# Kernel tuning notes

Hardware: AMD Instinct MI355X
Metric: run time of the kernel (lower is better)

Reference implementation:

```python
import jax, jax.numpy as jnp
import numpy as np

H = 256          # hidden_size
TH_X = 0.05      # delta threshold on inputs
TH_H = 0.05      # delta threshold on hidden state
F_IN = 6         # engineered feature count


def hardswish(v):
    return v * jnp.clip(v + 3.0, 0.0, 6.0) / 6.0


def setup_inputs() -> dict:
    key = jax.random.key(0)
    ks = jax.random.split(key, 6)
    B, T = 32, 4096
    x = jax.random.normal(ks[0], (B, T, 2), dtype=jnp.float32)
    # x2h: Linear(6, 3H, bias=False) -> weight (3H, 6)
    Wx = jax.random.normal(ks[1], (3 * H, F_IN), dtype=jnp.float32) * (1.0 / np.sqrt(F_IN))
    # h2h: Linear(H, 3H, bias=False) -> weight (3H, H)
    Wh = jax.random.normal(ks[2], (3 * H, H), dtype=jnp.float32) * (1.0 / np.sqrt(H))
    # fc_out: Linear(H, 2, bias=False)
    Wo = jax.random.normal(ks[3], (2, H), dtype=jnp.float32) * (1.0 / np.sqrt(H))
    # tcn conv1: Conv1d(2, 3, k=3, padding=16, dilation=16, bias=False) -> (O,I,K)=(3,2,3)
    Wc1 = jax.random.normal(ks[4], (3, 2, 3), dtype=jnp.float32) * 0.3
    # tcn conv2: Conv1d(3, 2, k=1) -> (2,3,1)
    Wc2 = jax.random.normal(ks[5], (2, 3, 1), dtype=jnp.float32) * 0.3
    return {"x": x, "Wx": Wx, "Wh": Wh, "Wo": Wo, "Wc1": Wc1, "Wc2": Wc2}


def _delta_gru(feats_TBF, Wx, Wh):
    # feats_TBF: (T, B, 6). Initial states are always zeros (the torch module
    # resets them whenever x_p_0 is None, which DeltaGRUModel always passes).
    T, B, F = feats_TBF.shape
    dt = feats_TBF.dtype
    carry0 = (
        jnp.zeros((B, F), dt),        # x_p
        jnp.zeros((B, H), dt),        # h
        jnp.zeros((B, H), dt),        # h_p
        jnp.zeros((B, H), dt),        # dm_nh
        jnp.zeros((B, 3 * H), dt),    # dm
    )

    def step(carry, xt):
        x_p, h, h_p, dm_nh, dm = carry
        dx = xt - x_p
        dh = h - h_p
        dxa = jnp.abs(dx)
        dha = jnp.abs(dh)
        dx = jnp.where(dxa < TH_X, 0.0, dx)
        dh = jnp.where(dha < TH_H, 0.0, dh)
        x_p = jnp.where(dxa >= TH_X, xt, x_p)
        h_p = jnp.where(dha >= TH_H, h, h_p)
        mac_x = dx @ Wx.T + dm          # (B, 3H)
        mac_h = dh @ Wh.T               # (B, 3H)
        mxr, mxz, mxn = jnp.split(mac_x, 3, axis=1)
        mhr, mhz, mhn = jnp.split(mac_h, 3, axis=1)
        dm_r = mxr + mhr
        dm_z = mxz + mhz
        dm_n = mxn
        dm_nh = mhn + dm_nh
        dm = jnp.concatenate([dm_r, dm_z, dm_n], axis=1)
        r = jax.nn.sigmoid(dm_r)
        z = jax.nn.sigmoid(dm_z)
        n = jnp.tanh(dm_n + r * dm_nh)
        h = (1.0 - z) * n + z * h
        return (x_p, h, h_p, dm_nh, dm), h

    _, hs = jax.lax.scan(step, carry0, feats_TBF)  # hs: (T, B, H)
    return hs


def reference(x, Wx, Wh, Wo, Wc1, Wc2):
    # x: (B, T, 2)
    B, T, _ = x.shape
    # --- TCN skip path ---
    xc = jnp.transpose(x, (0, 2, 1))  # (B, 2, T)
    c1 = jax.lax.conv_general_dilated(
        xc, Wc1, window_strides=(1,), padding=[(16, 16)], rhs_dilation=(16,),
        dimension_numbers=("NCH", "OIH", "NCH"))
    c2 = jax.lax.conv_general_dilated(
        hardswish(c1), Wc2, window_strides=(1,), padding=[(0, 0)],
        dimension_numbers=("NCH", "OIH", "NCH"))
    skip = jnp.transpose(hardswish(c2), (0, 2, 1))  # (B, T, 2)
    # --- engineered features ---
    i = x[..., 0:1]
    q = x[..., 1:2]
    amp2 = i * i + q * q
    amp = jnp.sqrt(jnp.maximum(amp2, 1e-12))
    amp3 = amp * amp2
    i_prev = jnp.pad(i[:, :-1, :], ((0, 0), (1, 0), (0, 0)))
    q_prev = jnp.pad(q[:, :-1, :], ((0, 0), (1, 0), (0, 0)))
    feats = jnp.concatenate([i, q, amp, amp3, i_prev, q_prev], axis=-1)  # (B,T,6)
    # --- delta-GRU scan (time-major) ---
    hs = _delta_gru(jnp.transpose(feats, (1, 0, 2)), Wx, Wh)  # (T, B, H)
    out = jnp.transpose(hs, (1, 0, 2))  # (B, T, H)
    return out @ Wo.T + skip  # (B, T, 2)
```

## Files before the change

kernel.cpp:

```cpp
#include <hip/hip_runtime.h>
#include <math.h>

#define HH 256
#define FIN 6
#define TT 4096
#define BB 32
#define TH 0.05f

typedef _Float16 h2 __attribute__((ext_vector_type(2)));
struct H8 { h2 a, b, c, d; };

__device__ __forceinline__ float hswish(float v) {
    float c = fminf(fmaxf(v + 3.0f, 0.0f), 6.0f);
    return v * c * (1.0f / 6.0f);
}
__device__ __forceinline__ float fexp2(float x) { return __builtin_amdgcn_exp2f(x); }
__device__ __forceinline__ float frcp(float x)  { return __builtin_amdgcn_rcpf(x); }
__device__ __forceinline__ float sigm(float x)  { return frcp(1.0f + fexp2(-1.44269504f * x)); }
__device__ __forceinline__ float tanhf_fast(float x) {
    float ax = fabsf(x);
    float e = fexp2(2.88539008f * ax);
    float t = 1.0f - 2.0f * frcp(e + 1.0f);
    return copysignf(t, x);
}

__device__ __forceinline__ float dpp_row_sum16(float p) {
    int x = __float_as_int(p);
    p += __int_as_float(__builtin_amdgcn_update_dpp(0, x, 0x118, 0xF, 0xF, true));
    x = __float_as_int(p);
    p += __int_as_float(__builtin_amdgcn_update_dpp(0, x, 0x114, 0xF, 0xF, true));
    x = __float_as_int(p);
    p += __int_as_float(__builtin_amdgcn_update_dpp(0, x, 0x112, 0xF, 0xF, true));
    x = __float_as_int(p);
    p += __int_as_float(__builtin_amdgcn_update_dpp(0, x, 0x111, 0xF, 0xF, true));
    return p;
}

__global__ __launch_bounds__(256) void k_prep(
        const float* __restrict__ x, const float* __restrict__ Wc1,
        const float* __restrict__ Wc2, float* __restrict__ feats,
        float* __restrict__ out) {
    int idx = blockIdx.x * 256 + threadIdx.x;
    if (idx >= BB * TT) return;
    int b = idx >> 12;
    int t = idx & (TT - 1);
    const float* xb = x + (size_t)b * TT * 2;
    float i0 = xb[t * 2 + 0], q0 = xb[t * 2 + 1];
    float ip = (t > 0) ? xb[(t - 1) * 2 + 0] : 0.0f;
    float qp = (t > 0) ? xb[(t - 1) * 2 + 1] : 0.0f;
    float amp2 = i0 * i0 + q0 * q0;
    float amp  = sqrtf(fmaxf(amp2, 1e-12f));
    float amp3 = amp * amp2;
    float* f = feats + (size_t)idx * 6;
    f[0] = i0; f[1] = q0; f[2] = amp; f[3] = amp3; f[4] = ip; f[5] = qp;

    float c1[3];
#pragma unroll
    for (int m = 0; m < 3; m++) {
        float acc = 0.0f;
#pragma unroll
        for (int k = 0; k < 3; k++) {
            int tt = t + (k - 1) * 16;
            if (tt >= 0 && tt < TT) {
                acc += Wc1[m * 6 + 0 * 3 + k] * xb[tt * 2 + 0];
                acc += Wc1[m * 6 + 1 * 3 + k] * xb[tt * 2 + 1];
            }
        }
        c1[m] = hswish(acc);
    }
#pragma unroll
    for (int o = 0; o < 2; o++) {
        float acc = Wc2[o * 3 + 0] * c1[0] + Wc2[o * 3 + 1] * c1[1] + Wc2[o * 3 + 2] * c1[2];
        out[(size_t)idx * 2 + o] = hswish(acc);
    }
}

__global__ __launch_bounds__(1024) void k_gru(
        const float* __restrict__ feats, const float* __restrict__ Wx,
        const float* __restrict__ Wh, const float* __restrict__ Wo,
        float* __restrict__ out) {
    __shared__ float s_out[TT * 2];
    __shared__ __align__(16) _Float16 s_dhh[2][HH];
    __shared__ __align__(16) float s_dx[2][8];
    __shared__ float s_feat[2][128 * FIN];

    const int tid  = threadIdx.x;
    const int wv   = tid >> 6;
    const int lane = tid & 63;
    const int q    = lane >> 4;
    const int row  = wv * 16 + (lane & 15);
    const int b    = blockIdx.x;
    const float* fb = feats + (size_t)b * TT * FIN;

    for (int i = tid; i < TT * 2; i += 1024) s_out[i] = 0.0f;
    for (int i = tid; i < 128 * FIN; i += 1024) s_feat[0][i] = fb[i];
    if (tid < 4) s_dx[tid >> 1][6 + (tid & 1)] = 0.0f;

    h2 wr[32], wz[32], wn[32];
    {
        const int k0 = q * 64;
        const float4* p0 = (const float4*)(Wh + (size_t)(0 * HH + row) * HH + k0);
        const float4* p1 = (const float4*)(Wh + (size_t)(1 * HH + row) * HH + k0);
        const float4* p2 = (const float4*)(Wh + (size_t)(2 * HH + row) * HH + k0);
#pragma unroll
        for (int c = 0; c < 16; c++) {
            float4 v0 = p0[c], v1 = p1[c], v2 = p2[c];
            wr[2 * c]     = h2{(_Float16)v0.x, (_Float16)v0.y};
            wr[2 * c + 1] = h2{(_Float16)v0.z, (_Float16)v0.w};
            wz[2 * c]     = h2{(_Float16)v1.x, (_Float16)v1.y};
            wz[2 * c + 1] = h2{(_Float16)v1.z, (_Float16)v1.w};
            wn[2 * c]     = h2{(_Float16)v2.x, (_Float16)v2.y};
            wn[2 * c + 1] = h2{(_Float16)v2.z, (_Float16)v2.w};
        }
    }
    float wxr0 = 0.0f, wxr1 = 0.0f, wxz0 = 0.0f, wxz1 = 0.0f, wxn0 = 0.0f, wxn1 = 0.0f;
    if (q < 3) {
        wxr0 = Wx[(size_t)(0 * HH + row) * FIN + 2 * q];
        wxr1 = Wx[(size_t)(0 * HH + row) * FIN + 2 * q + 1];
        wxz0 = Wx[(size_t)(1 * HH + row) * FIN + 2 * q];
        wxz1 = Wx[(size_t)(1 * HH + row) * FIN + 2 * q + 1];
        wxn0 = Wx[(size_t)(2 * HH + row) * FIN + 2 * q];
        wxn1 = Wx[(size_t)(2 * HH + row) * FIN + 2 * q + 1];
    }
    const float woc = (q < 2) ? Wo[q * HH + row] : 0.0f;

    float h = 0.0f, hp = 0.0f, dmr = 0.0f, dmz = 0.0f, dmn = 0.0f, dmnh = 0.0f;
    float xp = 0.0f, curf = 0.0f;
    if (tid < FIN) curf = fb[tid];

    __syncthreads();

    for (int t = 0; t < TT; t++) {
        const int tb = t & 1;

        if ((t & 127) == 64 && t + 64 < TT) {
            const int w = (t >> 7) + 1;
            for (int i = tid; i < 128 * FIN; i += 1024)
                s_feat[w & 1][i] = fb[(size_t)w * 128 * FIN + i];
        }

        {
            float dh = h - hp;
            bool keep = fabsf(dh) >= TH;
            if (q == 0) s_dhh[tb][row] = (_Float16)(keep ? dh : 0.0f);
            if (keep) hp = h;
        }
        if (tid < FIN) {
            float dx = curf - xp;
            bool keep = fabsf(dx) >= TH;
            s_dx[tb][tid] = keep ? dx : 0.0f;
            if (keep) xp = curf;
        }
        __syncthreads();

        float ar, az, an, axn;
        {
            const float2 dxp = *((const float2*)s_dx[tb] + q);
            ar  = fmaf(dxp.x, wxr0, dxp.y * wxr1);
            az  = fmaf(dxp.x, wxz0, dxp.y * wxz1);
            axn = fmaf(dxp.x, wxn0, dxp.y * wxn1);
            an  = 0.0f;
        }
        {
            const H8* dp = (const H8*)s_dhh[tb] + q * 8;
#pragma unroll
            for (int c = 0; c < 8; c++) {
                H8 d = dp[c];
                ar = __builtin_amdgcn_fdot2(d.a, wr[4 * c + 0], ar, false);
                az = __builtin_amdgcn_fdot2(d.a, wz[4 * c + 0], az, false);
                an = __builtin_amdgcn_fdot2(d.a, wn[4 * c + 0], an, false);
                ar = __builtin_amdgcn_fdot2(d.b, wr[4 * c + 1], ar, false);
                az = __builtin_amdgcn_fdot2(d.b, wz[4 * c + 1], az, false);
                an = __builtin_amdgcn_fdot2(d.b, wn[4 * c + 1], an, false);
                ar = __builtin_amdgcn_fdot2(d.c, wr[4 * c + 2], ar, false);
                az = __builtin_amdgcn_fdot2(d.c, wz[4 * c + 2], az, false);
                an = __builtin_amdgcn_fdot2(d.c, wn[4 * c + 2], an, false);
                ar = __builtin_amdgcn_fdot2(d.d, wr[4 * c + 3], ar, false);
                az = __builtin_amdgcn_fdot2(d.d, wz[4 * c + 3], az, false);
                an = __builtin_amdgcn_fdot2(d.d, wn[4 * c + 3], an, false);
            }
        }
        ar  += __shfl_xor(ar, 16, 64);  ar  += __shfl_xor(ar, 32, 64);
        az  += __shfl_xor(az, 16, 64);  az  += __shfl_xor(az, 32, 64);
        an  += __shfl_xor(an, 16, 64);  an  += __shfl_xor(an, 32, 64);
        axn += __shfl_xor(axn, 16, 64); axn += __shfl_xor(axn, 32, 64);

        dmr += ar;
        dmz += az;
        dmn += axn;
        dmnh += an;

        {
            float r = sigm(dmr);
            float z = sigm(dmz);
            float nn = tanhf_fast(dmn + r * dmnh);
            h = (1.0f - z) * nn + z * h;
        }

        {
            float p = h * woc;
            p = dpp_row_sum16(p);
            if ((lane & 15) == 15 && q < 2) atomicAdd(&s_out[2 * t + q], p);
        }

        if (tid < FIN && t + 1 < TT) {
            const int tn = t + 1;
            curf = s_feat[(tn >> 7) & 1][(tn & 127) * FIN + tid];
        }
    }

    __syncthreads();
    const size_t outbase = (size_t)b * TT * 2;
    for (int i = tid; i < TT * 2; i += 1024) out[outbase + i] += s_out[i];
}

extern "C" void kernel_launch(void* const* d_in, const int* in_sizes, int n_in,
                              void* d_out, int out_size, void* d_ws, size_t ws_size,
                              hipStream_t stream) {
    const float* x   = (const float*)d_in[0];
    const float* Wx  = (const float*)d_in[1];
    const float* Wh  = (const float*)d_in[2];
    const float* Wo  = (const float*)d_in[3];
    const float* Wc1 = (const float*)d_in[4];
    const float* Wc2 = (const float*)d_in[5];
    float* out = (float*)d_out;
    float* feats = (float*)d_ws;

    k_prep<<<(BB * TT + 255) / 256, 256, 0, stream>>>(x, Wc1, Wc2, feats, out);
    k_gru<<<BB, 1024, 0, stream>>>(feats, Wx, Wh, Wo, out);
}
```

Before: 6.161 ms.

## Halve GRU block to 512 threads with Wz in LDS and Wn streamed from global

Result: faster. 5.169 ms (-16.1%).

```diff
diff --git a/kernel.cpp b/kernel.cpp
--- a/kernel.cpp
+++ b/kernel.cpp
@@ -8,7 +8,7 @@
 #define TH 0.05f
 
 typedef _Float16 h2 __attribute__((ext_vector_type(2)));
-struct H8 { h2 a, b, c, d; };
+struct __align__(16) H8 { h2 a, b, c, d; };
 
 __device__ __forceinline__ float hswish(float v) {
     float c = fminf(fmaxf(v + 3.0f, 0.0f), 6.0f);
@@ -75,74 +75,99 @@
     }
 }
 
-__global__ __launch_bounds__(1024) void k_gru(
+__global__ __launch_bounds__(256) void k_pack(
+        const float* __restrict__ Wh, _Float16* __restrict__ zp,
+        _Float16* __restrict__ np) {
+    int id = blockIdx.x * 256 + threadIdx.x;
+    if (id >= 16384) return;
+    int which = id >> 13;
+    int c     = (id >> 9) & 15;
+    int slice = id & 511;
+    int row = slice & 255, half = slice >> 8;
+    int g = 1 + which;
+    const float* src = Wh + ((size_t)(g * HH + row)) * HH + half * 128 + 8 * c;
+    _Float16* dst = (which ? np : zp) + ((size_t)c * 512 + slice) * 8;
+#pragma unroll
+    for (int j = 0; j < 8; j++) dst[j] = (_Float16)src[j];
+}
+
+#define CH(CC, NR) { H8 zw_ = zl[(CC) * 512]; H8 dd_ = dp[CC];                 \
+    ar0 = __builtin_amdgcn_fdot2(dd_.a, wr[4 * (CC) + 0], ar0, false);         \
+    az0 = __builtin_amdgcn_fdot2(dd_.a, zw_.a, az0, false);                    \
+    an0 = __builtin_amdgcn_fdot2(dd_.a, NR.a, an0, false);                     \
+    ar1 = __builtin_amdgcn_fdot2(dd_.b, wr[4 * (CC) + 1], ar1, false);         \
+    az1 = __builtin_amdgcn_fdot2(dd_.b, zw_.b, az1, false);                    \
+    an1 = __builtin_amdgcn_fdot2(dd_.b, NR.b, an1, false);                     \
+    ar0 = __builtin_amdgcn_fdot2(dd_.c, wr[4 * (CC) + 2], ar0, false);         \
+    az0 = __builtin_amdgcn_fdot2(dd_.c, zw_.c, az0, false);                    \
+    an0 = __builtin_amdgcn_fdot2(dd_.c, NR.c, an0, false);                     \
+    ar1 = __builtin_amdgcn_fdot2(dd_.d, wr[4 * (CC) + 3], ar1, false);         \
+    az1 = __builtin_amdgcn_fdot2(dd_.d, zw_.d, az1, false);                    \
+    an1 = __builtin_amdgcn_fdot2(dd_.d, NR.d, an1, false); }
+
+__global__ __launch_bounds__(512) void k_gru(
         const float* __restrict__ feats, const float* __restrict__ Wx,
         const float* __restrict__ Wh, const float* __restrict__ Wo,
+        const _Float16* __restrict__ zp, const _Float16* __restrict__ np,
         float* __restrict__ out) {
-    __shared__ float s_out[TT * 2];
+    extern __shared__ __align__(16) _Float16 z_lds[];
     __shared__ __align__(16) _Float16 s_dhh[2][HH];
     __shared__ __align__(16) float s_dx[2][8];
-    __shared__ float s_feat[2][128 * FIN];
 
     const int tid  = threadIdx.x;
     const int wv   = tid >> 6;
     const int lane = tid & 63;
-    const int q    = lane >> 4;
-    const int row  = wv * 16 + (lane & 15);
+    const int half = lane >> 5;
+    const int row  = wv * 32 + (lane & 31);
+    const int slice = half * 256 + row;
     const int b    = blockIdx.x;
     const float* fb = feats + (size_t)b * TT * FIN;
-
-    for (int i = tid; i < TT * 2; i += 1024) s_out[i] = 0.0f;
-    for (int i = tid; i < 128 * FIN; i += 1024) s_feat[0][i] = fb[i];
-    if (tid < 4) s_dx[tid >> 1][6 + (tid & 1)] = 0.0f;
-
-    h2 wr[32], wz[32], wn[32];
+    float* outb = out + (size_t)b * TT * 2;
+
+    for (int i = tid; i < 8192; i += 512)
+        ((float4*)z_lds)[i] = ((const float4*)zp)[i];
+
+    h2 wr[64];
     {
-        const int k0 = q * 64;
-        const float4* p0 = (const float4*)(Wh + (size_t)(0 * HH + row) * HH + k0);
-        const float4* p1 = (const float4*)(Wh + (size_t)(1 * HH + row) * HH + k0);
-        const float4* p2 = (const float4*)(Wh + (size_t)(2 * HH + row) * HH + k0);
-#pragma unroll
-        for (int c = 0; c < 16; c++) {
-            float4 v0 = p0[c], v1 = p1[c], v2 = p2[c];
+        const float4* p0 = (const float4*)(Wh + (size_t)(0 * HH + row) * HH + half * 128);
+#pragma unroll
+        for (int c = 0; c < 32; c++) {
+            float4 v0 = p0[c];
             wr[2 * c]     = h2{(_Float16)v0.x, (_Float16)v0.y};
             wr[2 * c + 1] = h2{(_Float16)v0.z, (_Float16)v0.w};
-            wz[2 * c]     = h2{(_Float16)v1.x, (_Float16)v1.y};
-            wz[2 * c + 1] = h2{(_Float16)v1.z, (_Float16)v1.w};
-            wn[2 * c]     = h2{(_Float16)v2.x, (_Float16)v2.y};
-            wn[2 * c + 1] = h2{(_Float16)v2.z, (_Float16)v2.w};
-        }
-    }
-    float wxr0 = 0.0f, wxr1 = 0.0f, wxz0 = 0.0f, wxz1 = 0.0f, wxn0 = 0.0f, wxn1 = 0.0f;
-    if (q < 3) {
-        wxr0 = Wx[(size_t)(0 * HH + row) * FIN + 2 * q];
-        wxr1 = Wx[(size_t)(0 * HH + row) * FIN + 2 * q + 1];
-        wxz0 = Wx[(size_t)(1 * HH + row) * FIN + 2 * q];
-        wxz1 = Wx[(size_t)(1 * HH + row) * FIN + 2 * q + 1];
-        wxn0 = Wx[(size_t)(2 * HH + row) * FIN + 2 * q];
-        wxn1 = Wx[(size_t)(2 * HH + row) * FIN + 2 * q + 1];
-    }
-    const float woc = (q < 2) ? Wo[q * HH + row] : 0.0f;
+        }
+    }
+    float wxr0, wxr1, wxr2, wxz0, wxz1, wxz2, wxn0, wxn1, wxn2;
+    {
+        const int f0 = 3 * half;
+        wxr0 = Wx[(size_t)(0 * HH + row) * FIN + f0];
+        wxr1 = Wx[(size_t)(0 * HH + row) * FIN + f0 + 1];
+        wxr2 = Wx[(size_t)(0 * HH + row) * FIN + f0 + 2];
+        wxz0 = Wx[(size_t)(1 * HH + row) * FIN + f0];
+        wxz1 = Wx[(size_t)(1 * HH + row) * FIN + f0 + 1];
+        wxz2 = Wx[(size_t)(1 * HH + row) * FIN + f0 + 2];
+        wxn0 = Wx[(size_t)(2 * HH + row) * FIN + f0];
+        wxn1 = Wx[(size_t)(2 * HH + row) * FIN + f0 + 1];
+        wxn2 = Wx[(size_t)(2 * HH + row) * FIN + f0 + 2];
+    }
+    const float woc = Wo[half * HH + row];
 
     float h = 0.0f, hp = 0.0f, dmr = 0.0f, dmz = 0.0f, dmn = 0.0f, dmnh = 0.0f;
     float xp = 0.0f, curf = 0.0f;
     if (tid < FIN) curf = fb[tid];
 
+    const H8* zl = (const H8*)z_lds + slice;
+    const H8* nl = (const H8*)np + slice;
+
     __syncthreads();
 
     for (int t = 0; t < TT; t++) {
         const int tb = t & 1;
 
-        if ((t & 127) == 64 && t + 64 < TT) {
-            const int w = (t >> 7) + 1;
-            for (int i = tid; i < 128 * FIN; i += 1024)
-                s_feat[w & 1][i] = fb[(size_t)w * 128 * FIN + i];
-        }
-
         {
             float dh = h - hp;
             bool keep = fabsf(dh) >= TH;
-            if (q == 0) s_dhh[tb][row] = (_Float16)(keep ? dh : 0.0f);
+            if (half == 0) s_dhh[tb][row] = (_Float16)(keep ? dh : 0.0f);
             if (keep) hp = h;
         }
         if (tid < FIN) {
@@ -153,37 +178,29 @@
         }
         __syncthreads();
 
-        float ar, az, an, axn;
-        {
-            const float2 dxp = *((const float2*)s_dx[tb] + q);
-            ar  = fmaf(dxp.x, wxr0, dxp.y * wxr1);
-            az  = fmaf(dxp.x, wxz0, dxp.y * wxz1);
-            axn = fmaf(dxp.x, wxn0, dxp.y * wxn1);
-            an  = 0.0f;
-        }
-        {
-            const H8* dp = (const H8*)s_dhh[tb] + q * 8;
-#pragma unroll
-            for (int c = 0; c < 8; c++) {
-                H8 d = dp[c];
-                ar = __builtin_amdgcn_fdot2(d.a, wr[4 * c + 0], ar, false);
-                az = __builtin_amdgcn_fdot2(d.a, wz[4 * c + 0], az, false);
-                an = __builtin_amdgcn_fdot2(d.a, wn[4 * c + 0], an, false);
-                ar = __builtin_amdgcn_fdot2(d.b, wr[4 * c + 1], ar, false);
-                az = __builtin_amdgcn_fdot2(d.b, wz[4 * c + 1], az, false);
-                an = __builtin_amdgcn_fdot2(d.b, wn[4 * c + 1], an, false);
-                ar = __builtin_amdgcn_fdot2(d.c, wr[4 * c + 2], ar, false);
-                az = __builtin_amdgcn_fdot2(d.c, wz[4 * c + 2], az, false);
-                an = __builtin_amdgcn_fdot2(d.c, wn[4 * c + 2], an, false);
-                ar = __builtin_amdgcn_fdot2(d.d, wr[4 * c + 3], ar, false);
-                az = __builtin_amdgcn_fdot2(d.d, wz[4 * c + 3], az, false);
-                an = __builtin_amdgcn_fdot2(d.d, wn[4 * c + 3], an, false);
-            }
-        }
-        ar  += __shfl_xor(ar, 16, 64);  ar  += __shfl_xor(ar, 32, 64);
-        az  += __shfl_xor(az, 16, 64);  az  += __shfl_xor(az, 32, 64);
-        an  += __shfl_xor(an, 16, 64);  an  += __shfl_xor(an, 32, 64);
-        axn += __shfl_xor(axn, 16, 64); axn += __shfl_xor(axn, 32, 64);
+        float dxa = s_dx[tb][3 * half], dxb = s_dx[tb][3 * half + 1],
+              dxc = s_dx[tb][3 * half + 2];
+        float ar0 = fmaf(dxa, wxr0, fmaf(dxb, wxr1, dxc * wxr2));
+        float az0 = fmaf(dxa, wxz0, fmaf(dxb, wxz1, dxc * wxz2));
+        float axn = fmaf(dxa, wxn0, fmaf(dxb, wxn1, dxc * wxn2));
+        float ar1 = 0.0f, az1 = 0.0f, an0 = 0.0f, an1 = 0.0f;
+
+        const H8* dp = (const H8*)s_dhh[tb] + half * 16;
+        {
+            H8 na0 = nl[0 * 512],  na1 = nl[1 * 512],  na2 = nl[2 * 512],  na3 = nl[3 * 512];
+            H8 nb0 = nl[4 * 512],  nb1 = nl[5 * 512],  nb2 = nl[6 * 512],  nb3 = nl[7 * 512];
+            CH(0, na0) CH(1, na1) CH(2, na2) CH(3, na3)
+            na0 = nl[8 * 512];  na1 = nl[9 * 512];  na2 = nl[10 * 512]; na3 = nl[11 * 512];
+            CH(4, nb0) CH(5, nb1) CH(6, nb2) CH(7, nb3)
+            nb0 = nl[12 * 512]; nb1 = nl[13 * 512]; nb2 = nl[14 * 512]; nb3 = nl[15 * 512];
+            CH(8, na0) CH(9, na1) CH(10, na2) CH(11, na3)
+            CH(12, nb0) CH(13, nb1) CH(14, nb2) CH(15, nb3)
+        }
+        float ar = ar0 + ar1, az = az0 + az1, an = an0 + an1;
+        ar  += __shfl_xor(ar, 32, 64);
+        az  += __shfl_xor(az, 32, 64);
+        an  += __shfl_xor(an, 32, 64);
+        axn += __shfl_xor(axn, 32, 64);
 
         dmr += ar;
         dmz += az;
@@ -199,19 +216,13 @@
 
         {
             float p = h * woc;
+            p += __shfl_xor(p, 16, 64);
             p = dpp_row_sum16(p);
-            if ((lane & 15) == 15 && q < 2) atomicAdd(&s_out[2 * t + q], p);
-        }
-
-        if (tid < FIN && t + 1 < TT) {
-            const int tn = t + 1;
-            curf = s_feat[(tn >> 7) & 1][(tn & 127) * FIN + tid];
-        }
-    }
-
-    __syncthreads();
-    const size_t outbase = (size_t)b * TT * 2;
-    for (int i = tid; i < TT * 2; i += 1024) out[outbase + i] += s_out[i];
+            if ((lane & 31) == 31) atomicAdd(&outb[2 * t + half], p);
+        }
+
+        if (tid < FIN && t + 1 < TT) curf = fb[(size_t)(t + 1) * FIN + tid];
+    }
 }
 
 extern "C" void kernel_launch(void* const* d_in, const int* in_sizes, int n_in,
@@ -225,7 +236,12 @@
     const float* Wc2 = (const float*)d_in[5];
     float* out = (float*)d_out;
     float* feats = (float*)d_ws;
+    _Float16* zp = (_Float16*)((char*)d_ws + 3145728);
+    _Float16* np = (_Float16*)((char*)d_ws + 3145728 + 131072);
 
     k_prep<<<(BB * TT + 255) / 256, 256, 0, stream>>>(x, Wc1, Wc2, feats, out);
-    k_gru<<<BB, 1024, 0, stream>>>(feats, Wx, Wh, Wo, out);
-}
+    k_pack<<<64, 256, 0, stream>>>(Wh, zp, np);
+    hipFuncSetAttribute(reinterpret_cast<const void*>(k_gru),
+                        hipFuncAttributeMaxDynamicSharedMemorySize, 131072);
+    k_gru<<<BB, 512, 131072, stream>>>(feats, Wx, Wh, Wo, zp, np, out);
+}
```
